# Performance work log

Hardware: AMD Instinct MI355X
Metric: run time of the kernel (lower is better)

The kernel has to match this reference:

```python
import jax, jax.numpy as jnp
import numpy as np

N = 128            # codeword length (power of 2)
LIST = 8           # SCL list size
L2 = 2 * LIST      # decoders kept during path expansion
STAGES = 7         # log2(N)
LLR_MAX = 30.0
BATCH = 2048
FROZEN_POS = np.arange(N // 2)
FROZEN_IND = np.zeros(N, dtype=bool)
FROZEN_IND[FROZEN_POS] = True
INFO_POS = np.setdiff1d(np.arange(N), FROZEN_POS)


def _cn_op(x, y):
    # min-sum boxplus with LLR clipping
    x = jnp.clip(x, -LLR_MAX, LLR_MAX)
    y = jnp.clip(y, -LLR_MAX, LLR_MAX)
    return jnp.sign(x) * jnp.sign(y) * jnp.minimum(jnp.abs(x), jnp.abs(y))


def _vn_op(x, y, u):
    return (1.0 - 2.0 * u) * x + y


def _leaf(state, i):
    # Update single bit i across all 2L decoders, update path metrics,
    # and for info bits sort + duplicate the best L paths.
    uhat, llr, pm, ptr, bidx = state
    frozen = bool(FROZEN_IND[i])
    if not frozen:
        # set bit=1 for the upper half of decoders (path expansion)
        u_slice = uhat[:, :, 0, i]
        u_slice = u_slice.at[bidx[:, None], ptr[:, LIST:]].set(1.0)
        uhat = uhat.at[:, :, 0, i].set(u_slice)
    # path metric update, Eq.(10) of Stimming et al.
    u = jnp.take_along_axis(uhat[:, :, 0, i], ptr, axis=1)
    l = jnp.clip(jnp.take_along_axis(llr[:, :, 0, i], ptr, axis=1), -LLR_MAX, LLR_MAX)
    pm = pm + jax.nn.softplus(-(1.0 - 2.0 * u) * l)
    if not frozen:
        order = jnp.argsort(pm, axis=-1)
        pm = jnp.take_along_axis(pm, order, axis=1)
        ptr = jnp.take_along_axis(ptr, order, axis=1)
        lo = ptr[:, :LIST]
        up = ptr[:, LIST:]
        uhat = uhat.at[bidx[:, None], up].set(uhat[bidx[:, None], lo])
        llr = llr.at[bidx[:, None], up].set(llr[bidx[:, None], lo])
        pm = pm.at[:, LIST:].set(pm[:, :LIST])
    return (uhat, llr, pm, ptr, bidx)


def _decode(state, start, length):
    # recursive SCL tree traversal over contiguous index block [start, start+length)
    if length == 1:
        return _leaf(state, start)
    s = int(np.log2(length))
    h = length // 2
    uhat, llr, pm, ptr, bidx = state
    lsl = slice(start, start + h)
    rsl = slice(start + h, start + length)
    # f (check-node) update -> left child
    f = _cn_op(llr[:, :, s, lsl], llr[:, :, s, rsl])
    llr = llr.at[:, :, s - 1, lsl].set(f)
    uhat, llr, pm, ptr, bidx = _decode((uhat, llr, pm, ptr, bidx), start, h)
    # g (variable-node) update -> right child
    g = _vn_op(llr[:, :, s, lsl], llr[:, :, s, rsl], uhat[:, :, s - 1, lsl])
    llr = llr.at[:, :, s - 1, rsl].set(g)
    uhat, llr, pm, ptr, bidx = _decode((uhat, llr, pm, ptr, bidx), start + h, h)
    # combine partial sums: left XOR right, right pass-through
    ul = uhat[:, :, s - 1, lsl]
    ur = uhat[:, :, s - 1, rsl]
    ux = ul + ur - 2.0 * ul * ur  # XOR for {0,1} values (differentiable form)
    uhat = uhat.at[:, :, s, start:start + length].set(jnp.concatenate([ux, ur], axis=-1))
    return (uhat, llr, pm, ptr, bidx)


def setup_inputs() -> dict:
    key = jax.random.key(0)
    inputs = 2.0 * jax.random.normal(key, (BATCH, N), dtype=jnp.float32)
    return {"inputs": inputs}


def reference(inputs):
    bs = inputs.shape[0]
    llr_ch = -inputs.astype(jnp.float32)  # logits -> LLR sign convention
    uhat = jnp.zeros((bs, L2, STAGES + 1, N), jnp.float32)
    llr = jnp.zeros((bs, L2, STAGES + 1, N), jnp.float32)
    llr = llr.at[:, :, STAGES, :].set(llr_ch[:, None, :])
    pm = jnp.zeros((bs, L2), jnp.float32)
    pm = pm.at[:, 1:LIST].set(LLR_MAX).at[:, LIST + 1:].set(LLR_MAX)
    ptr = jnp.tile(jnp.arange(L2)[None, :], (bs, 1))
    bidx = jnp.arange(bs)
    uhat, llr, pm, ptr, _ = _decode((uhat, llr, pm, ptr, bidx), 0, N)
    # final sort and de-permutation of the list dimension
    order = jnp.argsort(pm, axis=-1)
    pm = jnp.take_along_axis(pm, order, axis=1)
    ptr = jnp.take_along_axis(ptr, order, axis=1)
    uhat = uhat[bidx[:, None], ptr]
    cand = jnp.argmin(pm, axis=-1)
    c_hat = uhat[bidx, cand, 0, :]       # [bs, n] best codeword estimate
    return c_hat[:, INFO_POS]            # [bs, k] info bits
```

## Files before the change

### kernel.cpp

```cpp
#include <hip/hip_runtime.h>
#include <math.h>

#define LMAX 30.0f
typedef unsigned long long ull;
typedef unsigned int u32;

__device__ __forceinline__ float clip30(float x) { return fminf(fmaxf(x, -LMAX), LMAX); }
__device__ __forceinline__ float cnop(float x, float y) {
    x = clip30(x); y = clip30(y);
    const float m = fminf(fabsf(x), fabsf(y));
    const unsigned sg = (__float_as_uint(x) ^ __float_as_uint(y)) & 0x80000000u;
    return __uint_as_float(__float_as_uint(m) | sg);
}

#define SWZI(x, PAT) __builtin_amdgcn_ds_swizzle((x), (PAT))
#define SWZF(x, PAT) __int_as_float(__builtin_amdgcn_ds_swizzle(__float_as_int(x), (PAT)))

template<int CTRL>
__device__ __forceinline__ int dppi(int x) {
    return __builtin_amdgcn_update_dpp(x, x, CTRL, 0xF, 0xF, false);
}
template<int CTRL>
__device__ __forceinline__ float dppf(float x) {
    return __int_as_float(dppi<CTRL>(__float_as_int(x)));
}
#define CTL_XOR8 0x128
#define CTL_XOR2 0x4E
#define CTL_XOR1 0xB1

#if __has_builtin(__builtin_amdgcn_permlane16_swap)
typedef int v2j_ __attribute__((ext_vector_type(2)));
__device__ __forceinline__ int swap16i(int x) {
    v2j_ r = __builtin_amdgcn_permlane16_swap(x, x, false, false);
    return (r[0] != x) ? r[0] : r[1];
}
#else
__device__ __forceinline__ int swap16i(int x) { return SWZI(x, 0x401F); }
#endif
__device__ __forceinline__ float swap16f(float x) { return __int_as_float(swap16i(__float_as_int(x))); }

__device__ __forceinline__ float gfb(float v, int a) {
    return __int_as_float(__builtin_amdgcn_ds_bpermute(a, __float_as_int(v)));
}
__device__ __forceinline__ ull bperm64b(ull v, int a) {
    const int lo = __builtin_amdgcn_ds_bpermute(a, (int)(u32)v);
    const int hi = __builtin_amdgcn_ds_bpermute(a, (int)(u32)(v >> 32));
    return ((ull)(u32)hi << 32) | (u32)lo;
}

__device__ __forceinline__ u32 enc2(u32 w)  { w ^= (w >> 1) & 0x1u; return w; }
__device__ __forceinline__ u32 enc4(u32 w)  { w ^= (w >> 1) & 0x5u; w ^= (w >> 2) & 0x3u; return w; }
__device__ __forceinline__ u32 enc8(u32 w)  { w ^= (w >> 1) & 0x55u; w ^= (w >> 2) & 0x33u;
                                              w ^= (w >> 4) & 0x0fu; return w; }
__device__ __forceinline__ u32 enc16(u32 w) { w ^= (w >> 1) & 0x5555u; w ^= (w >> 2) & 0x3333u;
                                              w ^= (w >> 4) & 0x0f0fu; w ^= (w >> 8) & 0x00ffu; return w; }
__device__ __forceinline__ u32 enc32(u32 w) { w ^= (w >> 1) & 0x55555555u; w ^= (w >> 2) & 0x33333333u;
                                              w ^= (w >> 4) & 0x0f0f0f0fu; w ^= (w >> 8) & 0x00ff00ffu;
                                              w ^= (w >> 16) & 0x0000ffffu; return w; }

#define F6_() { _Pragma("unroll") for (int k = 0; k < 16; ++k) S5[k] = cnop(C[k], C[k + 16]); }
#define G6_(II) { const u32 ub = enc32((u32)(uh >> ((II) - 96))); \
    _Pragma("unroll") for (int k = 0; k < 16; ++k) { \
        const int u = (ub >> (q + 2 * k)) & 1; \
        S5[k] = u ? (C[k + 16] - C[k]) : (C[k + 16] + C[k]); } }
#define F5_() { _Pragma("unroll") for (int k = 0; k < 8; ++k) S4[k] = cnop(S5[k], S5[k + 8]); }
#define G5_(II) { const u32 ub = enc16((u32)(uh >> ((II) - 80)) & 0xffffu); \
    _Pragma("unroll") for (int k = 0; k < 8; ++k) { \
        const int u = (ub >> (q + 2 * k)) & 1; \
        S4[k] = u ? (S5[k + 8] - S5[k]) : (S5[k + 8] + S5[k]); } }
#define F4_() { _Pragma("unroll") for (int k = 0; k < 4; ++k) S3[k] = cnop(S4[k], S4[k + 4]); }
#define G4_(II) { const u32 ub = enc8((u32)(uh >> ((II) - 72)) & 0xffu); \
    _Pragma("unroll") for (int k = 0; k < 4; ++k) { \
        const int u = (ub >> (q + 2 * k)) & 1; \
        S3[k] = u ? (S4[k + 4] - S4[k]) : (S4[k + 4] + S4[k]); } }
#define REPL2_(t0, t1) { \
    const float P0_ = swap16f(t0), P1_ = swap16f(t1); \
    R2[0] = q ? P0_ : (t0); R2[1] = q ? (t0) : P0_; \
    R2[2] = q ? P1_ : (t1); R2[3] = q ? (t1) : P1_; }
#define F3R_() { const float a0_ = cnop(S3[0], S3[2]); \
                 const float a1_ = cnop(S3[1], S3[3]); REPL2_(a0_, a1_); }
#define G3R_(II) { const u32 ub = enc4((u32)(uh >> ((II) - 68)) & 0xfu); \
    const int u0 = (ub >> q) & 1, u1 = (ub >> (q + 2)) & 1; \
    const float a0_ = u0 ? (S3[2] - S3[0]) : (S3[2] + S3[0]); \
    const float a1_ = u1 ? (S3[3] - S3[1]) : (S3[3] + S3[1]); REPL2_(a0_, a1_); }
#define F2_() { R1[0] = cnop(R2[0], R2[2]); R1[1] = cnop(R2[1], R2[3]); }
#define G2_(II) { const u32 ub = enc2((u32)(uh >> ((II) - 66)) & 3u); \
    R1[0] = (ub & 1) ? (R2[2] - R2[0]) : (R2[2] + R2[0]); \
    R1[1] = (ub & 2) ? (R2[3] - R2[1]) : (R2[3] + R2[1]); }

#define LEAF_(II, L0, DOCLONE) { \
    uh |= upBit << ((II) - 64); \
    const float l_ = clip30(L0); \
    const float tail_ = log1pf(expf(-fabsf(l_))); \
    pm += (isUp ? fmaxf(l_, 0.0f) : fmaxf(-l_, 0.0f)) + tail_; \
    int r_ = 0; \
    { \
        const u32 pmB = __float_as_uint(pm); \
        _Pragma("unroll") \
        for (int k = 0; k < 8; ++k) { \
            const u32 pmj = (u32)__builtin_amdgcn_ds_bpermute(A0 + 4 * k, __float_as_int(pm)); \
            r_ += ((pmj < pmB) || (pmj == pmB && (idx0 + k) < pos)) ? 1 : 0; \
        } \
    } \
    r_ += swap16i(r_); \
    rFinal = r_; \
    if (DOCLONE) { \
        const int inv_ = __builtin_amdgcn_ds_permute((r_ | gbase) << 2, pos); \
        const int p8_ = dppi<CTL_XOR8>(inv_); \
        const int ga_ = ((isUp ? p8_ : inv_) | gbase) << 2; \
        pm = gfb(pm, ga_); \
        uh = bperm64b(uh, ga_); \
        if ((((II) >> 0) & 1) == 0) { R1[0] = gfb(R1[0], ga_); R1[1] = gfb(R1[1], ga_); } \
        if ((((II) >> 1) & 1) == 0) { _Pragma("unroll") for (int e = 0; e < 4; ++e) \
                                      R2[e] = gfb(R2[e], ga_); } \
        if ((((II) >> 2) & 1) == 0) { _Pragma("unroll") for (int e = 0; e < 4; ++e) \
                                      S3[e] = gfb(S3[e], ga_); } \
        if ((((II) >> 3) & 1) == 0) { _Pragma("unroll") for (int e = 0; e < 8; ++e) \
                                      S4[e] = gfb(S4[e], ga_); } \
        if ((((II) >> 4) & 1) == 0) { _Pragma("unroll") for (int e = 0; e < 16; ++e) \
                                      S5[e] = gfb(S5[e], ga_); } \
    } \
}

#define RLF(x, J) __uint_as_float((u32)__builtin_amdgcn_readlane(__float_as_int(x), (J)))

__global__ __launch_bounds__(64) void scl_kernel(const float* __restrict__ in,
                                                 float* __restrict__ out) {
    __shared__ float chS[128];
    const int lane = threadIdx.x;
    const int w = lane & 31;
    const int d = lane >> 5;
    const int pos = lane & 15;
    const int q = (lane >> 4) & 1;
    const int gbase = lane & 48;
    const int dbase = lane & 32;
    const bool isUp = (lane & 8) != 0;
    const ull upBit = (ull)((lane >> 3) & 1);
    const int idx0 = q << 3;
    const int A0 = (dbase | (q << 3)) << 2;

    const size_t base = ((size_t)blockIdx.x * 2 + d) * 128;
    const float a1 = -in[base + w],      c1 = -in[base + 64 + w];
    const float a2 = -in[base + 32 + w], c2 = -in[base + 96 + w];
    chS[d * 64 + w] = a1 + c1;
    chS[d * 64 + 32 + w] = a2 + c2;
    __syncthreads();
    float C[32];
    #pragma unroll
    for (int k = 0; k < 32; ++k) C[k] = chS[d * 64 + q + 2 * k];

    float v1 = cnop(a1, c1), v2 = cnop(a2, c2);
    { const float n1 = cnop(v1, v2); v2 = v1 + v2; v1 = n1; }
    { const float o1 = swap16f(v1), o2 = swap16f(v2);
      v1 = (w & 16) ? (o1 + v1) : cnop(v1, o1);
      v2 = (w & 16) ? (o2 + v2) : cnop(v2, o2); }
    { const float o1 = dppf<CTL_XOR8>(v1), o2 = dppf<CTL_XOR8>(v2);
      v1 = (w & 8) ? (o1 + v1) : cnop(v1, o1);
      v2 = (w & 8) ? (o2 + v2) : cnop(v2, o2); }
    { const float o1 = SWZF(v1, 0x101F), o2 = SWZF(v2, 0x101F);
      v1 = (w & 4) ? (o1 + v1) : cnop(v1, o1);
      v2 = (w & 4) ? (o2 + v2) : cnop(v2, o2); }
    { const float o1 = dppf<CTL_XOR2>(v1), o2 = dppf<CTL_XOR2>(v2);
      v1 = (w & 2) ? (o1 + v1) : cnop(v1, o1);
      v2 = (w & 2) ? (o2 + v2) : cnop(v2, o2); }
    { const float o1 = dppf<CTL_XOR1>(v1), o2 = dppf<CTL_XOR1>(v2);
      v1 = (w & 1) ? (o1 + v1) : cnop(v1, o1);
      v2 = (w & 1) ? (o2 + v2) : cnop(v2, o2); }
    const float sp1 = fmaxf(-clip30(v1), 0.0f) + log1pf(expf(-fabsf(clip30(v1))));
    const float sp2 = fmaxf(-clip30(v2), 0.0f) + log1pf(expf(-fabsf(clip30(v2))));

    float pm = ((pos == 0) || (pos == 8)) ? 0.0f : LMAX;
    if (lane < 32) {
        #pragma unroll
        for (int j = 0; j < 32; ++j) pm += RLF(sp1, j);
        #pragma unroll
        for (int j = 0; j < 32; ++j) pm += RLF(sp2, j);
    } else {
        #pragma unroll
        for (int j = 32; j < 64; ++j) pm += RLF(sp1, j);
        #pragma unroll
        for (int j = 32; j < 64; ++j) pm += RLF(sp2, j);
    }

    float S5[16], S4[8], S3[4], R2[4], R1[2];
    ull uh = 0;
    int rFinal = 0;

    #pragma unroll 1
    for (int ie = 64; ie < 128; ie += 2) {
        {
            const int ii = ie;
            const int t = __builtin_ctz(ii);
            switch (t) {
                case 1: { G2_(ii); } break;
                case 2: { G3R_(ii); F2_(); } break;
                case 3: { G4_(ii); F3R_(); F2_(); } break;
                case 4: { G5_(ii); F4_(); F3R_(); F2_(); } break;
                case 5: { G6_(ii); F5_(); F4_(); F3R_(); F2_(); } break;
                default: { F6_(); F5_(); F4_(); F3R_(); F2_(); } break;
            }
            const float l0 = cnop(R1[0], R1[1]);
            LEAF_(ii, l0, 1);
        }
        {
            const int ii = ie + 1;
            const int ug = (int)((uh >> (ii - 65)) & 1ULL);
            const float l0 = ug ? (R1[1] - R1[0]) : (R1[1] + R1[0]);
            LEAF_(ii, l0, (ii != 127));
        }
    }

    const ull m = __ballot(rFinal == 0);
    const int bl = dbase + (int)__builtin_ctz((u32)(m >> dbase));
    const ull uhB = bperm64b(uh, bl << 2);
    const size_t ob = ((size_t)blockIdx.x * 2 + d) * 64;
    out[ob + w] = (float)((uhB >> w) & 1ULL);
    out[ob + 32 + w] = (float)((uhB >> (w + 32)) & 1ULL);
}

extern "C" void kernel_launch(void* const* d_in, const int* in_sizes, int n_in,
                              void* d_out, int out_size, void* d_ws, size_t ws_size,
                              hipStream_t stream) {
    (void)n_in; (void)out_size; (void)d_ws; (void)ws_size;
    const float* in = (const float*)d_in[0];
    float* out = (float*)d_out;
    const int batch = in_sizes[0] / 128;
    scl_kernel<<<dim3(batch / 2), dim3(64), 0, stream>>>(in, out);
}
```

Measured before the change: 62.35 us.

## Fully unroll SCL leaf loop via templates and skip unneeded state permutes

Replaces the runtime leaf loop and switch with compile-time template recursion over all 64 info leaves, so each leaf's stage updates and clone permutes are resolved statically. The 64-bit path history is split into two 32-bit words, and the high word is only permuted once it can hold bits. Clone permutes of intermediate LLR buffers that are not yet live are skipped. This cuts bpermute traffic and loop/branch overhead, at the cost of much larger code size and possible instruction-cache or register pressure. An unused dummy leaf function is left in.

```diff
diff --git a/kernel.cpp b/kernel.cpp
--- a/kernel.cpp
+++ b/kernel.cpp
@@ -42,10 +42,15 @@
 __device__ __forceinline__ float gfb(float v, int a) {
     return __int_as_float(__builtin_amdgcn_ds_bpermute(a, __float_as_int(v)));
 }
-__device__ __forceinline__ ull bperm64b(ull v, int a) {
-    const int lo = __builtin_amdgcn_ds_bpermute(a, (int)(u32)v);
-    const int hi = __builtin_amdgcn_ds_bpermute(a, (int)(u32)(v >> 32));
-    return ((ull)(u32)hi << 32) | (u32)lo;
+__device__ __forceinline__ u32 gub(u32 v, int a) {
+    return (u32)__builtin_amdgcn_ds_bpermute(a, (int)v);
+}
+
+template<int LO>
+__device__ __forceinline__ u32 gbits(u32 lo, u32 hi) {
+    if constexpr (LO >= 32) return hi >> (LO - 32);
+    else if constexpr (LO == 0) return lo;
+    else return (lo >> LO) | (hi << (32 - LO));
 }
 
 __device__ __forceinline__ u32 enc2(u32 w)  { w ^= (w >> 1) & 0x1u; return w; }
@@ -58,68 +63,165 @@
                                               w ^= (w >> 4) & 0x0f0f0f0fu; w ^= (w >> 8) & 0x00ff00ffu;
                                               w ^= (w >> 16) & 0x0000ffffu; return w; }
 
-#define F6_() { _Pragma("unroll") for (int k = 0; k < 16; ++k) S5[k] = cnop(C[k], C[k + 16]); }
-#define G6_(II) { const u32 ub = enc32((u32)(uh >> ((II) - 96))); \
-    _Pragma("unroll") for (int k = 0; k < 16; ++k) { \
-        const int u = (ub >> (q + 2 * k)) & 1; \
-        S5[k] = u ? (C[k + 16] - C[k]) : (C[k + 16] + C[k]); } }
-#define F5_() { _Pragma("unroll") for (int k = 0; k < 8; ++k) S4[k] = cnop(S5[k], S5[k + 8]); }
-#define G5_(II) { const u32 ub = enc16((u32)(uh >> ((II) - 80)) & 0xffffu); \
-    _Pragma("unroll") for (int k = 0; k < 8; ++k) { \
-        const int u = (ub >> (q + 2 * k)) & 1; \
-        S4[k] = u ? (S5[k + 8] - S5[k]) : (S5[k + 8] + S5[k]); } }
-#define F4_() { _Pragma("unroll") for (int k = 0; k < 4; ++k) S3[k] = cnop(S4[k], S4[k + 4]); }
-#define G4_(II) { const u32 ub = enc8((u32)(uh >> ((II) - 72)) & 0xffu); \
-    _Pragma("unroll") for (int k = 0; k < 4; ++k) { \
-        const int u = (ub >> (q + 2 * k)) & 1; \
-        S3[k] = u ? (S4[k + 4] - S4[k]) : (S4[k + 4] + S4[k]); } }
-#define REPL2_(t0, t1) { \
-    const float P0_ = swap16f(t0), P1_ = swap16f(t1); \
-    R2[0] = q ? P0_ : (t0); R2[1] = q ? (t0) : P0_; \
-    R2[2] = q ? P1_ : (t1); R2[3] = q ? (t1) : P1_; }
-#define F3R_() { const float a0_ = cnop(S3[0], S3[2]); \
-                 const float a1_ = cnop(S3[1], S3[3]); REPL2_(a0_, a1_); }
-#define G3R_(II) { const u32 ub = enc4((u32)(uh >> ((II) - 68)) & 0xfu); \
-    const int u0 = (ub >> q) & 1, u1 = (ub >> (q + 2)) & 1; \
-    const float a0_ = u0 ? (S3[2] - S3[0]) : (S3[2] + S3[0]); \
-    const float a1_ = u1 ? (S3[3] - S3[1]) : (S3[3] + S3[1]); REPL2_(a0_, a1_); }
-#define F2_() { R1[0] = cnop(R2[0], R2[2]); R1[1] = cnop(R2[1], R2[3]); }
-#define G2_(II) { const u32 ub = enc2((u32)(uh >> ((II) - 66)) & 3u); \
-    R1[0] = (ub & 1) ? (R2[2] - R2[0]) : (R2[2] + R2[0]); \
-    R1[1] = (ub & 2) ? (R2[3] - R2[1]) : (R2[3] + R2[1]); }
-
-#define LEAF_(II, L0, DOCLONE) { \
-    uh |= upBit << ((II) - 64); \
-    const float l_ = clip30(L0); \
-    const float tail_ = log1pf(expf(-fabsf(l_))); \
-    pm += (isUp ? fmaxf(l_, 0.0f) : fmaxf(-l_, 0.0f)) + tail_; \
-    int r_ = 0; \
-    { \
-        const u32 pmB = __float_as_uint(pm); \
-        _Pragma("unroll") \
-        for (int k = 0; k < 8; ++k) { \
-            const u32 pmj = (u32)__builtin_amdgcn_ds_bpermute(A0 + 4 * k, __float_as_int(pm)); \
-            r_ += ((pmj < pmB) || (pmj == pmB && (idx0 + k) < pos)) ? 1 : 0; \
-        } \
-    } \
-    r_ += swap16i(r_); \
-    rFinal = r_; \
-    if (DOCLONE) { \
-        const int inv_ = __builtin_amdgcn_ds_permute((r_ | gbase) << 2, pos); \
-        const int p8_ = dppi<CTL_XOR8>(inv_); \
-        const int ga_ = ((isUp ? p8_ : inv_) | gbase) << 2; \
-        pm = gfb(pm, ga_); \
-        uh = bperm64b(uh, ga_); \
-        if ((((II) >> 0) & 1) == 0) { R1[0] = gfb(R1[0], ga_); R1[1] = gfb(R1[1], ga_); } \
-        if ((((II) >> 1) & 1) == 0) { _Pragma("unroll") for (int e = 0; e < 4; ++e) \
-                                      R2[e] = gfb(R2[e], ga_); } \
-        if ((((II) >> 2) & 1) == 0) { _Pragma("unroll") for (int e = 0; e < 4; ++e) \
-                                      S3[e] = gfb(S3[e], ga_); } \
-        if ((((II) >> 3) & 1) == 0) { _Pragma("unroll") for (int e = 0; e < 8; ++e) \
-                                      S4[e] = gfb(S4[e], ga_); } \
-        if ((((II) >> 4) & 1) == 0) { _Pragma("unroll") for (int e = 0; e < 16; ++e) \
-                                      S5[e] = gfb(S5[e], ga_); } \
-    } \
+struct Dec {
+    float C[32];
+    float S5[16], S4[8], S3[4], R2[4], R1[2];
+    float pm;
+    u32 uhLo, uhHi;
+    int rF;
+    int q, pos, gbase, A0, idx0;
+    u32 upB;
+    bool isUp;
+};
+
+__device__ __forceinline__ void f6(Dec& s) {
+    #pragma unroll
+    for (int k = 0; k < 16; ++k) s.S5[k] = cnop(s.C[k], s.C[k + 16]);
+}
+template<int II> __device__ __forceinline__ void g6(Dec& s) {
+    const u32 ub = enc32(gbits<II - 96>(s.uhLo, s.uhHi));
+    #pragma unroll
+    for (int k = 0; k < 16; ++k) {
+        const int u = (ub >> (s.q + 2 * k)) & 1;
+        s.S5[k] = u ? (s.C[k + 16] - s.C[k]) : (s.C[k + 16] + s.C[k]);
+    }
+}
+__device__ __forceinline__ void f5(Dec& s) {
+    #pragma unroll
+    for (int k = 0; k < 8; ++k) s.S4[k] = cnop(s.S5[k], s.S5[k + 8]);
+}
+template<int II> __device__ __forceinline__ void g5(Dec& s) {
+    const u32 ub = enc16(gbits<II - 80>(s.uhLo, s.uhHi) & 0xffffu);
+    #pragma unroll
+    for (int k = 0; k < 8; ++k) {
+        const int u = (ub >> (s.q + 2 * k)) & 1;
+        s.S4[k] = u ? (s.S5[k + 8] - s.S5[k]) : (s.S5[k + 8] + s.S5[k]);
+    }
+}
+__device__ __forceinline__ void f4(Dec& s) {
+    #pragma unroll
+    for (int k = 0; k < 4; ++k) s.S3[k] = cnop(s.S4[k], s.S4[k + 4]);
+}
+template<int II> __device__ __forceinline__ void g4(Dec& s) {
+    const u32 ub = enc8(gbits<II - 72>(s.uhLo, s.uhHi) & 0xffu);
+    #pragma unroll
+    for (int k = 0; k < 4; ++k) {
+        const int u = (ub >> (s.q + 2 * k)) & 1;
+        s.S3[k] = u ? (s.S4[k + 4] - s.S4[k]) : (s.S4[k + 4] + s.S4[k]);
+    }
+}
+__device__ __forceinline__ void repl2(Dec& s, float t0, float t1) {
+    const float P0 = swap16f(t0), P1 = swap16f(t1);
+    s.R2[0] = s.q ? P0 : t0; s.R2[1] = s.q ? t0 : P0;
+    s.R2[2] = s.q ? P1 : t1; s.R2[3] = s.q ? t1 : P1;
+}
+__device__ __forceinline__ void f3r(Dec& s) {
+    repl2(s, cnop(s.S3[0], s.S3[2]), cnop(s.S3[1], s.S3[3]));
+}
+template<int II> __device__ __forceinline__ void g3r(Dec& s) {
+    const u32 ub = enc4(gbits<II - 68>(s.uhLo, s.uhHi) & 0xfu);
+    const int u0 = (ub >> s.q) & 1, u1 = (ub >> (s.q + 2)) & 1;
+    repl2(s, u0 ? (s.S3[2] - s.S3[0]) : (s.S3[2] + s.S3[0]),
+             u1 ? (s.S3[3] - s.S3[1]) : (s.S3[3] + s.S3[1]));
+}
+__device__ __forceinline__ void f2(Dec& s) {
+    s.R1[0] = cnop(s.R2[0], s.R2[2]); s.R1[1] = cnop(s.R2[1], s.R2[3]);
+}
+template<int II> __device__ __forceinline__ void g2(Dec& s) {
+    const u32 ub = enc2(gbits<II - 66>(s.uhLo, s.uhHi) & 3u);
+    s.R1[0] = (ub & 1) ? (s.R2[2] - s.R2[0]) : (s.R2[2] + s.R2[0]);
+    s.R1[1] = (ub & 2) ? (s.R2[3] - s.R2[1]) : (s.R2[3] + s.R2[1]);
+}
+
+template<int II, bool CLONE>
+__device__ __forceinline__ void leaf(Dec& s, float l0) {
+    if constexpr (II - 64 < 32) s.uhLo |= s.upB << (II - 64);
+    else                        s.uhHi |= s.upB << (II - 96);
+    const float l = clip30(l0);
+    const float tail = log1pf(expf(-fabsf(l)));
+    s.pm += (s.isUp ? fmaxf(l, 0.0f) : fmaxf(-l, 0.0f)) + tail;
+    int r = 0;
+    {
+        const u32 pmB = __float_as_uint(s.pm);
+        #pragma unroll
+        for (int k = 0; k < 8; ++k) {
+            const u32 pmj = gub((u32)__float_as_int(s.pm) * 0u + (u32)0, 0) * 0u;
+        }
+    }
+    (void)r;
+}
+
+template<int II, bool CLONE>
+__device__ __forceinline__ void leafR(Dec& s, float l0) {
+    if constexpr (II - 64 < 32) s.uhLo |= s.upB << (II - 64);
+    else                        s.uhHi |= s.upB << (II - 96);
+    const float l = clip30(l0);
+    const float tail = log1pf(expf(-fabsf(l)));
+    s.pm += (s.isUp ? fmaxf(l, 0.0f) : fmaxf(-l, 0.0f)) + tail;
+    int r = 0;
+    {
+        const u32 pmB = __float_as_uint(s.pm);
+        #pragma unroll
+        for (int k = 0; k < 8; ++k) {
+            const u32 pmj = (u32)__builtin_amdgcn_ds_bpermute(s.A0 + 4 * k, __float_as_int(s.pm));
+            r += ((pmj < pmB) || (pmj == pmB && (s.idx0 + k) < s.pos)) ? 1 : 0;
+        }
+    }
+    r += swap16i(r);
+    s.rF = r;
+    if constexpr (CLONE) {
+        const int inv = __builtin_amdgcn_ds_permute((r | s.gbase) << 2, s.pos);
+        const int p8 = dppi<CTL_XOR8>(inv);
+        const int ga = ((s.isUp ? p8 : inv) | s.gbase) << 2;
+        s.pm = gfb(s.pm, ga);
+        s.uhLo = gub(s.uhLo, ga);
+        if constexpr (II >= 96) s.uhHi = gub(s.uhHi, ga);
+        if constexpr ((((II) >> 0) & 1) == 0 && II >= 66) {
+            s.R1[0] = gfb(s.R1[0], ga); s.R1[1] = gfb(s.R1[1], ga);
+        }
+        if constexpr ((((II) >> 1) & 1) == 0 && II >= 68) {
+            #pragma unroll
+            for (int e = 0; e < 4; ++e) s.R2[e] = gfb(s.R2[e], ga);
+        }
+        if constexpr ((((II) >> 2) & 1) == 0 && II >= 72) {
+            #pragma unroll
+            for (int e = 0; e < 4; ++e) s.S3[e] = gfb(s.S3[e], ga);
+        }
+        if constexpr ((((II) >> 3) & 1) == 0 && II >= 80) {
+            #pragma unroll
+            for (int e = 0; e < 8; ++e) s.S4[e] = gfb(s.S4[e], ga);
+        }
+        if constexpr ((((II) >> 4) & 1) == 0 && II >= 96) {
+            #pragma unroll
+            for (int e = 0; e < 16; ++e) s.S5[e] = gfb(s.S5[e], ga);
+        }
+    }
+}
+
+template<int II> __device__ __forceinline__ void evenLeaf(Dec& s) {
+    constexpr int t = (II == 64) ? 6 : __builtin_ctz(II);
+    if constexpr (t >= 6) f6(s);
+    if constexpr (t == 5) g6<II>(s);
+    if constexpr (t >= 5) f5(s);
+    if constexpr (t == 4) g5<II>(s);
+    if constexpr (t >= 4) f4(s);
+    if constexpr (t == 3) g4<II>(s);
+    if constexpr (t >= 3) f3r(s);
+    if constexpr (t == 2) g3r<II>(s);
+    if constexpr (t >= 2) f2(s);
+    if constexpr (t == 1) g2<II>(s);
+    const float l0 = cnop(s.R1[0], s.R1[1]);
+    leafR<II, true>(s, l0);
+}
+template<int II> __device__ __forceinline__ void oddLeaf(Dec& s) {
+    const int ug = (int)(gbits<II - 65>(s.uhLo, s.uhHi) & 1u);
+    const float l0 = ug ? (s.R1[1] - s.R1[0]) : (s.R1[1] + s.R1[0]);
+    leafR<II, (II != 127)>(s, l0);
+}
+template<int II> __device__ __forceinline__ void runPairs(Dec& s) {
+    evenLeaf<II>(s);
+    oddLeaf<II + 1>(s);
+    if constexpr (II + 2 < 128) runPairs<II + 2>(s);
 }
 
 #define RLF(x, J) __uint_as_float((u32)__builtin_amdgcn_readlane(__float_as_int(x), (J)))
@@ -130,14 +232,17 @@
     const int lane = threadIdx.x;
     const int w = lane & 31;
     const int d = lane >> 5;
-    const int pos = lane & 15;
-    const int q = (lane >> 4) & 1;
-    const int gbase = lane & 48;
     const int dbase = lane & 32;
-    const bool isUp = (lane & 8) != 0;
-    const ull upBit = (ull)((lane >> 3) & 1);
-    const int idx0 = q << 3;
-    const int A0 = (dbase | (q << 3)) << 2;
+
+    Dec s;
+    s.pos = lane & 15;
+    s.q = (lane >> 4) & 1;
+    s.gbase = lane & 48;
+    s.isUp = (lane & 8) != 0;
+    s.upB = (u32)((lane >> 3) & 1);
+    s.idx0 = s.q << 3;
+    s.A0 = (dbase | (s.q << 3)) << 2;
+    s.uhLo = 0; s.uhHi = 0; s.rF = 0;
 
     const size_t base = ((size_t)blockIdx.x * 2 + d) * 128;
     const float a1 = -in[base + w],      c1 = -in[base + 64 + w];
@@ -145,9 +250,8 @@
     chS[d * 64 + w] = a1 + c1;
     chS[d * 64 + 32 + w] = a2 + c2;
     __syncthreads();
-    float C[32];
-    #pragma unroll
-    for (int k = 0; k < 32; ++k) C[k] = chS[d * 64 + q + 2 * k];
+    #pragma unroll
+    for (int k = 0; k < 32; ++k) s.C[k] = chS[d * 64 + s.q + 2 * k];
 
     float v1 = cnop(a1, c1), v2 = cnop(a2, c2);
     { const float n1 = cnop(v1, v2); v2 = v1 + v2; v1 = n1; }
@@ -169,50 +273,26 @@
     const float sp1 = fmaxf(-clip30(v1), 0.0f) + log1pf(expf(-fabsf(clip30(v1))));
     const float sp2 = fmaxf(-clip30(v2), 0.0f) + log1pf(expf(-fabsf(clip30(v2))));
 
-    float pm = ((pos == 0) || (pos == 8)) ? 0.0f : LMAX;
+    s.pm = ((s.pos == 0) || (s.pos == 8)) ? 0.0f : LMAX;
     if (lane < 32) {
         #pragma unroll
-        for (int j = 0; j < 32; ++j) pm += RLF(sp1, j);
-        #pragma unroll
-        for (int j = 0; j < 32; ++j) pm += RLF(sp2, j);
+        for (int j = 0; j < 32; ++j) s.pm += RLF(sp1, j);
+        #pragma unroll
+        for (int j = 0; j < 32; ++j) s.pm += RLF(sp2, j);
     } else {
         #pragma unroll
-        for (int j = 32; j < 64; ++j) pm += RLF(sp1, j);
-        #pragma unroll
-        for (int j = 32; j < 64; ++j) pm += RLF(sp2, j);
-    }
-
-    float S5[16], S4[8], S3[4], R2[4], R1[2];
-    ull uh = 0;
-    int rFinal = 0;
-
-    #pragma unroll 1
-    for (int ie = 64; ie < 128; ie += 2) {
-        {
-            const int ii = ie;
-            const int t = __builtin_ctz(ii);
-            switch (t) {
-                case 1: { G2_(ii); } break;
-                case 2: { G3R_(ii); F2_(); } break;
-                case 3: { G4_(ii); F3R_(); F2_(); } break;
-                case 4: { G5_(ii); F4_(); F3R_(); F2_(); } break;
-                case 5: { G6_(ii); F5_(); F4_(); F3R_(); F2_(); } break;
-                default: { F6_(); F5_(); F4_(); F3R_(); F2_(); } break;
-            }
-            const float l0 = cnop(R1[0], R1[1]);
-            LEAF_(ii, l0, 1);
-        }
-        {
-            const int ii = ie + 1;
-            const int ug = (int)((uh >> (ii - 65)) & 1ULL);
-            const float l0 = ug ? (R1[1] - R1[0]) : (R1[1] + R1[0]);
-            LEAF_(ii, l0, (ii != 127));
-        }
-    }
-
-    const ull m = __ballot(rFinal == 0);
+        for (int j = 32; j < 64; ++j) s.pm += RLF(sp1, j);
+        #pragma unroll
+        for (int j = 32; j < 64; ++j) s.pm += RLF(sp2, j);
+    }
+
+    runPairs<64>(s);
+
+    const ull m = __ballot(s.rF == 0);
     const int bl = dbase + (int)__builtin_ctz((u32)(m >> dbase));
-    const ull uhB = bperm64b(uh, bl << 2);
+    const u32 lo = gub(s.uhLo, bl << 2);
+    const u32 hi = gub(s.uhHi, bl << 2);
+    const ull uhB = ((ull)hi << 32) | lo;
     const size_t ob = ((size_t)blockIdx.x * 2 + d) * 64;
     out[ob + w] = (float)((uhB >> w) & 1ULL);
     out[ob + 32 + w] = (float)((uhB >> (w + 32)) & 1ULL);
```

New measurement: 53.43 us. -14.3%, faster.
